# Kernel tuning notes

Measured on AMD Instinct MI355X. Metric: run time of the kernel, lower is better.

Reference implementation:

```python
import jax, jax.numpy as jnp
import numpy as np
import math

D_MODEL = 1024
NUM_HEADS = 16
D_K = D_MODEL // NUM_HEADS
B, NQ, NK = 2, 2048, 2048


def setup_inputs() -> dict:
    key = jax.random.key(0)
    ks = jax.random.split(key, 14)
    s = 1.0 / math.sqrt(D_MODEL)
    inp = {
        "query": jax.random.normal(ks[0], (B, NQ, D_MODEL), jnp.float32),
        "key": jax.random.normal(ks[1], (B, NK, D_MODEL), jnp.float32),
        "value": jax.random.normal(ks[2], (B, NK, D_MODEL), jnp.float32),
        "mask": jax.random.randint(ks[3], (B, NK), 0, 2, jnp.int32),
        "attn_bias": jax.random.normal(ks[4], (B, NQ, NK), jnp.float32),
        "w_q": jax.random.normal(ks[5], (D_MODEL, D_MODEL), jnp.float32) * s,
        "b_q": jnp.zeros((D_MODEL,), jnp.float32),
        "w_k": jax.random.normal(ks[6], (D_MODEL, D_MODEL), jnp.float32) * s,
        "b_k": jnp.zeros((D_MODEL,), jnp.float32),
        "w_v": jax.random.normal(ks[7], (D_MODEL, D_MODEL), jnp.float32) * s,
        "b_v": jnp.zeros((D_MODEL,), jnp.float32),
        "w_o": jax.random.normal(ks[8], (D_MODEL, D_MODEL), jnp.float32) * s,
        "b_o": jnp.zeros((D_MODEL,), jnp.float32),
    }
    return inp


def reference(query, key, value, mask, attn_bias, w_q, b_q, w_k, b_k, w_v, b_v, w_o, b_o):
    # Linear projections (torch Linear: x @ W^T + b), reshape to [B, H, N, d_k]
    def proj(x, w, b, n):
        return (x @ w.T + b).reshape(x.shape[0], n, NUM_HEADS, D_K).transpose(0, 2, 1, 3)

    Q = proj(query, w_q, b_q, query.shape[1])   # [B,H,Nq,dk]
    K = proj(key, w_k, b_k, key.shape[1])       # [B,H,Nk,dk]
    V = proj(value, w_v, b_v, value.shape[1])   # [B,H,Nk,dk]

    scores = jnp.einsum("bhqd,bhkd->bhqk", Q, K) / math.sqrt(D_K)
    scores = scores + attn_bias[:, None, :, :]           # bias broadcast over heads
    pad = (mask[:, None, None, :] == 0)                   # [B,1,1,Nk]
    scores = jnp.where(pad, jnp.float32(-1e9), scores)
    attn = jax.nn.softmax(scores, axis=-1)                # dropout is identity (eval)
    out = jnp.einsum("bhqk,bhkd->bhqd", attn, V)          # [B,H,Nq,dk]
    out = out.transpose(0, 2, 1, 3).reshape(query.shape[0], query.shape[1], D_MODEL)
    return out @ w_o.T + b_o
```

## Files before the change

kernel.cpp:

```cpp
#include <hip/hip_runtime.h>


typedef short bf16x8 __attribute__((ext_vector_type(8)));
typedef short bf16x4 __attribute__((ext_vector_type(4)));
typedef float f32x4 __attribute__((ext_vector_type(4)));
typedef int i32x4 __attribute__((ext_vector_type(4)));
typedef unsigned short u16;
typedef unsigned short u16x8 __attribute__((ext_vector_type(8)));
typedef unsigned short u16x4 __attribute__((ext_vector_type(4)));

#define MFMA16(a, b, c) __builtin_amdgcn_mfma_f32_16x16x32_bf16((a), (b), (c), 0, 0, 0)
#define GLD16(gp, lp)                                                     \
  __builtin_amdgcn_global_load_lds(                                       \
      (const __attribute__((address_space(1))) void*)(gp),                \
      (__attribute__((address_space(3))) void*)(lp), 16, 0, 0)

#define WAITVM_BAR(N) asm volatile("s_waitcnt vmcnt(" #N ")\ns_barrier" ::: "memory")
#define BAR() asm volatile("s_barrier" ::: "memory")

#if __has_builtin(__builtin_amdgcn_exp2f)
#define EXP2(x) __builtin_amdgcn_exp2f(x)
#else
#define EXP2(x) exp2f(x)
#endif

__device__ __forceinline__ f32x4 MFMA_PV(bf16x4 a, bf16x4 b, f32x4 c) {
#if __has_builtin(__builtin_amdgcn_mfma_f32_16x16x16bf16_1k)
  return __builtin_amdgcn_mfma_f32_16x16x16bf16_1k(a, b, c, 0, 0, 0);
#else
  asm("v_mfma_f32_16x16x16_bf16 %0, %1, %2, %0" : "+v"(c) : "v"(a), "v"(b));
  return c;
#endif
}

__device__ __forceinline__ u16 f2bf(float f) {
  union { float f; unsigned u; } v; v.f = f;
  return (u16)((v.u + 0x7fffu + ((v.u >> 16) & 1u)) >> 16);
}
__device__ __forceinline__ unsigned pk2(float x, float y) {
  union { float f; unsigned u; } a, b;
  a.f = x; b.f = y;
  return ((a.u + 0x8000u) >> 16) | ((b.u + 0x8000u) & 0xffff0000u);
}

struct ConvDesc { const float* src; u16* dst; int n; };
struct ConvArgs { ConvDesc d[7]; };

__device__ __forceinline__ void biasprep_body(const float* __restrict__ bias,
                                              const int* __restrict__ mask,
                                              u16* __restrict__ out, int i) {
  const int o0 = i * 16;
  const int rowg = o0 >> 11;
  const int b = rowg >> 11;
  const int off = o0 & 2047;
  const int a = off >> 6, g = (off >> 4) & 3;
  const float* src = bias + (size_t)rowg * 2048 + a * 64 + g * 4;
  const int* msk = mask + b * 2048 + a * 64 + g * 4;
  u16x8 w0 = {}, w1 = {};
#pragma unroll
  for (int c = 0; c < 4; c++) {
    f32x4 v = *(const f32x4*)(src + c * 16);
    i32x4 m = *(const i32x4*)(msk + c * 16);
#pragma unroll
    for (int j = 0; j < 4; j++) {
      u16 val = (m[j] != 0) ? f2bf(v[j] * 1.44269504f) : (u16)0xFF80;
      if (c < 2) w0[c * 4 + j] = val;
      else       w1[(c - 2) * 4 + j] = val;
    }
  }
  *(u16x8*)(out + o0) = w0;
  *(u16x8*)(out + o0 + 8) = w1;
}

__global__ __launch_bounds__(256)
void k_prep(ConvArgs a, const float* __restrict__ bias,
            const int* __restrict__ mask, u16* __restrict__ bout) {
  if (blockIdx.y == 7) {
    biasprep_body(bias, mask, bout, blockIdx.x * 256 + threadIdx.x);
    return;
  }
  ConvDesc cd = a.d[blockIdx.y];
  int i = (blockIdx.x * 256 + threadIdx.x) * 8;
  if (i >= cd.n) return;
  const float4* s = (const float4*)(cd.src + i);
  float4 f0 = s[0], f1 = s[1];
  u16x8 o;
  o[0] = f2bf(f0.x); o[1] = f2bf(f0.y); o[2] = f2bf(f0.z); o[3] = f2bf(f0.w);
  o[4] = f2bf(f1.x); o[5] = f2bf(f1.y); o[6] = f2bf(f1.z); o[7] = f2bf(f1.w);
  *(u16x8*)(cd.dst + i) = o;
}

__global__ __launch_bounds__(256)
void k_biasprep(const float* __restrict__ bias, const int* __restrict__ mask,
                u16* __restrict__ out) {
  biasprep_body(bias, mask, out, blockIdx.x * 256 + threadIdx.x);
}

template <int MF>
__device__ __forceinline__ void gemm_impl(const u16* __restrict__ A,
                                          const u16* __restrict__ Bw,
                                          const float* __restrict__ bias,
                                          void* __restrict__ outp, int mode,
                                          float oscale) {
  __shared__ u16 As[2][MF * 1024];
  __shared__ u16 Bs[2][4096];
  const int tid = threadIdx.x;
  const int lane = tid & 63;
  const int wv = tid >> 6;
  const int wr = wv >> 1, wc = wv & 1;
  const int m0 = blockIdx.y * (MF * 32), n0 = blockIdx.x * 128;

  f32x4 acc[MF][4] = {};

  const int s0 = tid, s1 = 256 + tid;
  const int r0 = s0 >> 2, c0 = (s0 & 3) ^ (r0 & 3);
  const int r1 = s1 >> 2, c1 = (s1 & 3) ^ (r1 & 3);
  const u16* gA0 = A + (size_t)(m0 + r0) * 1024 + c0 * 8;
  const u16* gA1 = A + (size_t)(m0 + r1) * 1024 + c1 * 8;
  const u16* gB0 = Bw + (size_t)(n0 + r0) * 1024 + c0 * 8;
  const u16* gB1 = Bw + (size_t)(n0 + r1) * 1024 + c1 * 8;
  u16* lA0 = &As[0][(tid & ~63) * 8];
  u16* lB0 = &Bs[0][(tid & ~63) * 8];

  GLD16(gA0, lA0);
  if constexpr (MF == 4) GLD16(gA1, lA0 + 2048);
  GLD16(gB0, lB0);
  GLD16(gB1, lB0 + 2048);
  WAITVM_BAR(0);

#define GSTEP(BUF, K0)                                                     \
  {                                                                        \
    const int nk = ((K0) + 32) & 1023;                                     \
    GLD16(gA0 + nk, lA0 + ((BUF) ^ 1) * (MF * 1024));                      \
    if constexpr (MF == 4)                                                 \
      GLD16(gA1 + nk, lA0 + 2048 + ((BUF) ^ 1) * (MF * 1024));             \
    GLD16(gB0 + nk, lB0 + ((BUF) ^ 1) * 4096);                             \
    GLD16(gB1 + nk, lB0 + 2048 + ((BUF) ^ 1) * 4096);                      \
    if constexpr (MF == 4) { WAITVM_BAR(4); } else { WAITVM_BAR(3); }      \
    bf16x8 af[MF], bfr[4];                                                 \
    _Pragma("unroll")                                                      \
    for (int mi = 0; mi < MF; mi++) {                                      \
      int row = wr * (MF * 16) + mi * 16 + (lane & 15);                    \
      int byt = row * 64 + (((lane >> 4) * 16) ^ ((row & 3) << 4));        \
      af[mi] = *(const bf16x8*)((const char*)&As[BUF][0] + byt);           \
    }                                                                      \
    _Pragma("unroll")                                                      \
    for (int ni = 0; ni < 4; ni++) {                                       \
      int row = wc * 64 + ni * 16 + (lane & 15);                           \
      int byt = row * 64 + (((lane >> 4) * 16) ^ ((row & 3) << 4));        \
      bfr[ni] = *(const bf16x8*)((const char*)&Bs[BUF][0] + byt);          \
    }                                                                      \
    __builtin_amdgcn_s_setprio(1);                                         \
    _Pragma("unroll")                                                      \
    for (int mi = 0; mi < MF; mi++)                                        \
      _Pragma("unroll")                                                    \
      for (int ni = 0; ni < 4; ni++)                                       \
        acc[mi][ni] = MFMA16(af[mi], bfr[ni], acc[mi][ni]);                \
    __builtin_amdgcn_s_setprio(0);                                         \
    BAR();                                                                 \
  }

  for (int k0 = 0; k0 < 1024; k0 += 64) {
    GSTEP(0, k0)
    GSTEP(1, k0 + 32)
  }
#undef GSTEP

#pragma unroll
  for (int ni = 0; ni < 4; ni++) {
    int n = n0 + wc * 64 + ni * 16 + (lane & 15);
    float bv = bias[n];
#pragma unroll
    for (int mi = 0; mi < MF; mi++) {
      int mb = m0 + wr * (MF * 16) + mi * 16 + (lane >> 4) * 4;
      if (mode == 2) {
        float* O = (float*)outp;
#pragma unroll
        for (int r = 0; r < 4; r++)
          O[(size_t)(mb + r) * 1024 + n] = (acc[mi][ni][r] + bv) * oscale;
      } else if (mode == 0) {
        u16* O = (u16*)outp;
        int b = mb >> 11, q = mb & 2047;
        int h = n >> 6, dk = n & 63;
        size_t base = ((size_t)(b * 16 + h) * 2048 + q) * 64 + dk;
#pragma unroll
        for (int r = 0; r < 4; r++)
          O[base + (size_t)r * 64] = f2bf((acc[mi][ni][r] + bv) * oscale);
      } else {
        u16* O = (u16*)outp;
        int b = mb >> 11, kv = mb & 2047;
        int h = n >> 6, dk = n & 63;
        u16x4 pk;
#pragma unroll
        for (int r = 0; r < 4; r++) pk[r] = f2bf((acc[mi][ni][r] + bv) * oscale);
        *(u16x4*)((u16*)O + ((size_t)((b * 16 + h) * 64 + dk)) * 2048 + kv) = pk;
      }
    }
  }
}

struct GemmDesc { const u16* A; const u16* W; const float* bias; void* out;
                  int mode; float oscale; };
struct Gemm3 { GemmDesc d[3]; };

__global__ __launch_bounds__(256, 2) void k_gemm_qkv(Gemm3 g3) {
  GemmDesc gd = g3.d[blockIdx.z];
  gemm_impl<4>(gd.A, gd.W, gd.bias, gd.out, gd.mode, gd.oscale);
}
__global__ __launch_bounds__(256, 2)
void k_gemm_o(const u16* __restrict__ A, const u16* __restrict__ W,
              const float* __restrict__ bias, float* __restrict__ out) {
  gemm_impl<2>(A, W, bias, out, 2, 1.0f);
}

__global__ __launch_bounds__(512, 4)
void k_attn(const u16* __restrict__ Qb, const u16* __restrict__ Kb,
            const u16* __restrict__ Vt, const u16* __restrict__ BiasE,
            u16* __restrict__ Ob) {
  __shared__ u16 Ks[2][128 * 64];
  __shared__ u16 Vs[2][64 * 128];

  const int tid = threadIdx.x, lane = tid & 63, w = tid >> 6;
  const int g = lane >> 4, q = lane & 15;
  const int bid = blockIdx.x;
  const int xcd = bid & 7, rr = bid >> 3;
  const int qt = rr & 15;
  const int pr = xcd + 8 * (rr >> 4);
  const int b = pr >> 4, h = pr & 15;
  const int q0 = qt * 128;
  const size_t bh = (size_t)(b * 16 + h);

  const u16* Qrow = Qb + (bh * 2048 + q0 + w * 16 + q) * 64;
  bf16x8 bq0 = *(const bf16x8*)(Qrow + g * 8);
  bf16x8 bq1 = *(const bf16x8*)(Qrow + 32 + g * 8);

  f32x4 acc[4] = {};
  float mrun = -1e30f, lrun = 0.f;

  const int sK1 = tid + 512;
  const int rK0 = tid >> 3, cK0 = (tid & 7) ^ (rK0 & 7);
  const int rK1 = sK1 >> 3, cK1 = (sK1 & 7) ^ (rK1 & 7);
  const int rV0 = tid >> 4, cV0 = (tid & 15) ^ (rV0 & 7);
  const int rV1 = sK1 >> 4, cV1 = (sK1 & 15) ^ (rV1 & 7);
  const u16* Kg = Kb + bh * 2048 * 64;
  const u16* Vg = Vt + bh * 64 * 2048;
  const int ld0 = (tid & ~63) * 8, ld1 = ld0 + 4096;

  const u16* brow = BiasE + ((size_t)b * 2048 + q0 + w * 16 + q) * 2048 + g * 16;

  GLD16(Kg + (size_t)rK0 * 64 + cK0 * 8, &Ks[0][ld0]);
  GLD16(Kg + (size_t)rK1 * 64 + cK1 * 8, &Ks[0][ld1]);
  GLD16(Vg + (size_t)rV0 * 2048 + cV0 * 8, &Vs[0][ld0]);
  GLD16(Vg + (size_t)rV1 * 2048 + cV1 * 8, &Vs[0][ld1]);
  u16x8 bb0 = *(const u16x8*)(brow);
  u16x8 bb1 = *(const u16x8*)(brow + 8);
  u16x8 bb2 = *(const u16x8*)(brow + 64);
  u16x8 bb3 = *(const u16x8*)(brow + 72);

#define ATTN_STEP(BUF, T)                                                      \
  {                                                                            \
    WAITVM_BAR(0);            \
    f32x4 sc[8];                                                               \
    __builtin_amdgcn_s_setprio(1);                                             \
    _Pragma("unroll")                                                          \
    for (int c = 0; c < 8; c++) {                                              \
      const int kvr = c * 16 + q;                                              \
      bf16x8 ak0 = *(const bf16x8*)((const char*)&Ks[BUF][0] + kvr * 128 +     \
                                    ((g * 16) ^ ((kvr & 7) << 4)));            \
      bf16x8 ak1 = *(const bf16x8*)((const char*)&Ks[BUF][0] + kvr * 128 +     \
                                    ((64 + g * 16) ^ ((kvr & 7) << 4)));       \
      const u16x8 blo = (c & 4) ? bb2 : bb0;                                   \
      const u16x8 bhi = (c & 4) ? bb3 : bb1;                                   \
      f32x4 cin;                                                               \
      _Pragma("unroll")                                                        \
      for (int r = 0; r < 4; r++) {                                            \
        unsigned braw = (unsigned)(((c & 3) < 2)                               \
                                       ? blo[(c & 3) * 4 + r]                  \
                                       : bhi[((c & 3) - 2) * 4 + r]);          \
        cin[r] = __uint_as_float(braw << 16);                                  \
      }                                                                        \
      f32x4 z = MFMA16(ak0, bq0, cin);                                         \
      sc[c] = MFMA16(ak1, bq1, z);                                             \
    }                                                                          \
    __builtin_amdgcn_s_setprio(0);                                             \
    const int nkv = (((T) + 1) & 15) * 128;                                    \
    GLD16(Kg + (size_t)(nkv + rK0) * 64 + cK0 * 8, &Ks[(BUF) ^ 1][ld0]);       \
    GLD16(Kg + (size_t)(nkv + rK1) * 64 + cK1 * 8, &Ks[(BUF) ^ 1][ld1]);       \
    GLD16(Vg + (size_t)rV0 * 2048 + nkv + cV0 * 8, &Vs[(BUF) ^ 1][ld0]);       \
    GLD16(Vg + (size_t)rV1 * 2048 + nkv + cV1 * 8, &Vs[(BUF) ^ 1][ld1]);       \
    bb0 = *(const u16x8*)(brow + nkv);                                         \
    bb1 = *(const u16x8*)(brow + nkv + 8);                                     \
    bb2 = *(const u16x8*)(brow + nkv + 64);                                    \
    bb3 = *(const u16x8*)(brow + nkv + 72);                                    \
    float tmax = -3e38f;                                                       \
    _Pragma("unroll")                                                          \
    for (int c = 0; c < 8; c++)                                                \
      _Pragma("unroll")                                                        \
      for (int r = 0; r < 4; r++) tmax = fmaxf(tmax, sc[c][r]);                \
    tmax = fmaxf(tmax, __shfl_xor(tmax, 16, 64));                              \
    tmax = fmaxf(tmax, __shfl_xor(tmax, 32, 64));                              \
    if (__any(tmax > mrun)) {                                                  \
      float mnew = fmaxf(mrun, tmax);                                          \
      float alpha = EXP2(mrun - mnew);                                         \
      mrun = mnew;                                                             \
      lrun *= alpha;                                                           \
      _Pragma("unroll")                                                        \
      for (int j = 0; j < 4; j++) {                                            \
        float aj = __shfl(alpha, g * 4 + j, 64);                               \
        _Pragma("unroll")                                                      \
        for (int d = 0; d < 4; d++) acc[d][j] *= aj;                           \
      }                                                                        \
    }                                                                          \
    float rsum = 0.f;                                                          \
    float pp[8][4];                                                            \
    _Pragma("unroll")                                                          \
    for (int c = 0; c < 8; c++)                                                \
      _Pragma("unroll")                                                        \
      for (int r = 0; r < 4; r++) {                                            \
        pp[c][r] = EXP2(sc[c][r] - mrun);                                      \
        rsum += pp[c][r];                                                      \
      }                                                                        \
    rsum += __shfl_xor(rsum, 16, 64);                                          \
    rsum += __shfl_xor(rsum, 32, 64);                                          \
    lrun += rsum;                                                              \
    __builtin_amdgcn_s_setprio(1);                                             \
    _Pragma("unroll")                                                          \
    for (int c = 0; c < 8; c++) {                                              \
      union { unsigned u[2]; bf16x4 v; } pa;                                   \
      pa.u[0] = pk2(pp[c][0], pp[c][1]);                                       \
      pa.u[1] = pk2(pp[c][2], pp[c][3]);                                       \
      _Pragma("unroll")                                                        \
      for (int d = 0; d < 4; d++) {                                            \
        const int dr = d * 16 + q;                                             \
        bf16x4 vb = *(const bf16x4*)((const char*)&Vs[BUF][0] + dr * 256 +     \
                                     ((c * 32 + g * 8) ^ ((dr & 7) << 4)));    \
        acc[d] = MFMA_PV(pa.v, vb, acc[d]);                                    \
      }                                                                        \
    }                                                                          \
    __builtin_amdgcn_s_setprio(0);                                             \
  }

  for (int t = 0; t < 16; t += 2) {
    ATTN_STEP(0, t)
    ATTN_STEP(1, t + 1)
  }
#undef ATTN_STEP

  float linv = 1.0f / lrun;
#pragma unroll
  for (int j = 0; j < 4; j++) {
    float li = __shfl(linv, g * 4 + j, 64);
    int qq = q0 + w * 16 + g * 4 + j;
#pragma unroll
    for (int d = 0; d < 4; d++)
      Ob[((size_t)b * 2048 + qq) * 1024 + h * 64 + d * 16 + q] =
          f2bf(acc[d][j] * li);
  }
}

extern "C" void kernel_launch(void* const* d_in, const int* in_sizes, int n_in,
                              void* d_out, int out_size, void* d_ws,
                              size_t ws_size, hipStream_t stream) {
  (void)in_sizes; (void)n_in; (void)out_size;
  const float* q_in = (const float*)d_in[0];
  const float* k_in = (const float*)d_in[1];
  const float* v_in = (const float*)d_in[2];
  const int* mask = (const int*)d_in[3];
  const float* attn_bias = (const float*)d_in[4];
  const float* w_q = (const float*)d_in[5];
  const float* b_q = (const float*)d_in[6];
  const float* w_k = (const float*)d_in[7];
  const float* b_k = (const float*)d_in[8];
  const float* w_v = (const float*)d_in[9];
  const float* b_v = (const float*)d_in[10];
  const float* w_o = (const float*)d_in[11];
  const float* b_o = (const float*)d_in[12];

  const size_t MB = 1u << 20;
  char* ws = (char*)d_ws;
  u16* XQ = (u16*)(ws + 0 * MB);
  u16* XK = (u16*)(ws + 8 * MB);
  u16* XV = (u16*)(ws + 16 * MB);
  u16* WQ = (u16*)(ws + 24 * MB);
  u16* WK = (u16*)(ws + 26 * MB);
  u16* WV = (u16*)(ws + 28 * MB);
  u16* WO = (u16*)(ws + 30 * MB);
  u16* Qb = (u16*)(ws + 32 * MB);
  u16* Kb = (u16*)(ws + 40 * MB);
  u16* Vt = (u16*)(ws + 48 * MB);
  u16* Ob = (u16*)(ws + 56 * MB);
  const bool merged = ws_size >= (size_t)80 * MB;
  u16* BiasE = (u16*)(ws + (merged ? 64 : 0) * MB);

  ConvArgs ca;
  ca.d[0] = {q_in, XQ, 4096 * 1024};
  ca.d[1] = {k_in, XK, 4096 * 1024};
  ca.d[2] = {v_in, XV, 4096 * 1024};
  ca.d[3] = {w_q, WQ, 1024 * 1024};
  ca.d[4] = {w_k, WK, 1024 * 1024};
  ca.d[5] = {w_v, WV, 1024 * 1024};
  ca.d[6] = {w_o, WO, 1024 * 1024};
  k_prep<<<dim3(2048, merged ? 8 : 7), 256, 0, stream>>>(ca, attn_bias, mask,
                                                         BiasE);

  const float QSCALE = 0.125f * 1.44269504f;
  Gemm3 g3;
  g3.d[0] = {XQ, WQ, b_q, (void*)Qb, 0, QSCALE};
  g3.d[1] = {XK, WK, b_k, (void*)Kb, 0, 1.0f};
  g3.d[2] = {XV, WV, b_v, (void*)Vt, 1, 1.0f};
  k_gemm_qkv<<<dim3(8, 32, 3), 256, 0, stream>>>(g3);

  if (!merged) k_biasprep<<<2048, 256, 0, stream>>>(attn_bias, mask, BiasE);

  k_attn<<<512, 512, 0, stream>>>(Qb, Kb, Vt, BiasE, Ob);

  k_gemm_o<<<dim3(8, 64), 256, 0, stream>>>(Ob, WO, b_o, (float*)d_out);
}
```

Baseline: 152.1 us.

## Switch attention kernel to 32x32x16 MFMA tiles with 4 waves per block

The attention kernel moves from 16x16 MFMA tiles to 32x32x16 bf16 MFMA. Each wave now owns 32 query rows, and the block shrinks to 256 threads. The P fragments are rearranged with v_permlane32_swap so they can feed the PV MFMA directly. The bias pre-layout is changed to match the new accumulator layout, and the output store is vectorized. This cuts cross-lane shuffles and LDS reads per FLOP, at the cost of more registers per wave and fewer waves per CU.

```diff
diff --git a/kernel.cpp b/kernel.cpp
--- a/kernel.cpp
+++ b/kernel.cpp
@@ -4,12 +4,14 @@
 typedef short bf16x8 __attribute__((ext_vector_type(8)));
 typedef short bf16x4 __attribute__((ext_vector_type(4)));
 typedef float f32x4 __attribute__((ext_vector_type(4)));
+typedef float f32x16 __attribute__((ext_vector_type(16)));
 typedef int i32x4 __attribute__((ext_vector_type(4)));
 typedef unsigned short u16;
 typedef unsigned short u16x8 __attribute__((ext_vector_type(8)));
 typedef unsigned short u16x4 __attribute__((ext_vector_type(4)));
 
 #define MFMA16(a, b, c) __builtin_amdgcn_mfma_f32_16x16x32_bf16((a), (b), (c), 0, 0, 0)
+#define MFMA32(a, b, c) __builtin_amdgcn_mfma_f32_32x32x16_bf16((a), (b), (c), 0, 0, 0)
 #define GLD16(gp, lp)                                                     \
   __builtin_amdgcn_global_load_lds(                                       \
       (const __attribute__((address_space(1))) void*)(gp),                \
@@ -24,15 +26,6 @@
 #define EXP2(x) exp2f(x)
 #endif
 
-__device__ __forceinline__ f32x4 MFMA_PV(bf16x4 a, bf16x4 b, f32x4 c) {
-#if __has_builtin(__builtin_amdgcn_mfma_f32_16x16x16bf16_1k)
-  return __builtin_amdgcn_mfma_f32_16x16x16bf16_1k(a, b, c, 0, 0, 0);
-#else
-  asm("v_mfma_f32_16x16x16_bf16 %0, %1, %2, %0" : "+v"(c) : "v"(a), "v"(b));
-  return c;
-#endif
-}
-
 __device__ __forceinline__ u16 f2bf(float f) {
   union { float f; unsigned u; } v; v.f = f;
   return (u16)((v.u + 0x7fffu + ((v.u >> 16) & 1u)) >> 16);
@@ -41,6 +34,9 @@
   union { float f; unsigned u; } a, b;
   a.f = x; b.f = y;
   return ((a.u + 0x8000u) >> 16) | ((b.u + 0x8000u) & 0xffff0000u);
+}
+__device__ __forceinline__ void pl32swap(unsigned& a, unsigned& b) {
+  asm("v_permlane32_swap_b32 %0, %1" : "+v"(a), "+v"(b));
 }
 
 struct ConvDesc { const float* src; u16* dst; int n; };
@@ -53,19 +49,20 @@
   const int rowg = o0 >> 11;
   const int b = rowg >> 11;
   const int off = o0 & 2047;
-  const int a = off >> 6, g = (off >> 4) & 3;
-  const float* src = bias + (size_t)rowg * 2048 + a * 64 + g * 4;
-  const int* msk = mask + b * 2048 + a * 64 + g * 4;
+  const int c = off >> 5;
+  const int hi = (off >> 4) & 1;
+  const float* src = bias + (size_t)rowg * 2048 + c * 32 + hi * 4;
+  const int* msk = mask + b * 2048 + c * 32 + hi * 4;
   u16x8 w0 = {}, w1 = {};
 #pragma unroll
-  for (int c = 0; c < 4; c++) {
-    f32x4 v = *(const f32x4*)(src + c * 16);
-    i32x4 m = *(const i32x4*)(msk + c * 16);
+  for (int t = 0; t < 4; t++) {
+    f32x4 v = *(const f32x4*)(src + t * 8);
+    i32x4 m = *(const i32x4*)(msk + t * 8);
 #pragma unroll
     for (int j = 0; j < 4; j++) {
       u16 val = (m[j] != 0) ? f2bf(v[j] * 1.44269504f) : (u16)0xFF80;
-      if (c < 2) w0[c * 4 + j] = val;
-      else       w1[(c - 2) * 4 + j] = val;
+      if (t < 2) w0[t * 4 + j] = val;
+      else       w1[(t - 2) * 4 + j] = val;
     }
   }
   *(u16x8*)(out + o0) = w0;
@@ -213,7 +210,7 @@
   gemm_impl<2>(A, W, bias, out, 2, 1.0f);
 }
 
-__global__ __launch_bounds__(512, 4)
+__global__ __launch_bounds__(256, 2)
 void k_attn(const u16* __restrict__ Qb, const u16* __restrict__ Kb,
             const u16* __restrict__ Vt, const u16* __restrict__ BiasE,
             u16* __restrict__ Ob) {
@@ -221,7 +218,7 @@
   __shared__ u16 Vs[2][64 * 128];
 
   const int tid = threadIdx.x, lane = tid & 63, w = tid >> 6;
-  const int g = lane >> 4, q = lane & 15;
+  const int l31 = lane & 31, hi2 = lane >> 5;
   const int bid = blockIdx.x;
   const int xcd = bid & 7, rr = bid >> 3;
   const int qt = rr & 15;
@@ -230,74 +227,87 @@
   const int q0 = qt * 128;
   const size_t bh = (size_t)(b * 16 + h);
 
-  const u16* Qrow = Qb + (bh * 2048 + q0 + w * 16 + q) * 64;
-  bf16x8 bq0 = *(const bf16x8*)(Qrow + g * 8);
-  bf16x8 bq1 = *(const bf16x8*)(Qrow + 32 + g * 8);
-
-  f32x4 acc[4] = {};
+  const u16* Qrow = Qb + (bh * 2048 + q0 + w * 32 + l31) * 64 + hi2 * 8;
+  bf16x8 bq[4];
+#pragma unroll
+  for (int dc = 0; dc < 4; dc++) bq[dc] = *(const bf16x8*)(Qrow + dc * 16);
+
+  f32x16 acc[2] = {};
   float mrun = -1e30f, lrun = 0.f;
 
-  const int sK1 = tid + 512;
-  const int rK0 = tid >> 3, cK0 = (tid & 7) ^ (rK0 & 7);
-  const int rK1 = sK1 >> 3, cK1 = (sK1 & 7) ^ (rK1 & 7);
-  const int rV0 = tid >> 4, cV0 = (tid & 15) ^ (rV0 & 7);
-  const int rV1 = sK1 >> 4, cV1 = (sK1 & 15) ^ (rV1 & 7);
   const u16* Kg = Kb + bh * 2048 * 64;
   const u16* Vg = Vt + bh * 64 * 2048;
-  const int ld0 = (tid & ~63) * 8, ld1 = ld0 + 4096;
-
-  const u16* brow = BiasE + ((size_t)b * 2048 + q0 + w * 16 + q) * 2048 + g * 16;
-
-  GLD16(Kg + (size_t)rK0 * 64 + cK0 * 8, &Ks[0][ld0]);
-  GLD16(Kg + (size_t)rK1 * 64 + cK1 * 8, &Ks[0][ld1]);
-  GLD16(Vg + (size_t)rV0 * 2048 + cV0 * 8, &Vs[0][ld0]);
-  GLD16(Vg + (size_t)rV1 * 2048 + cV1 * 8, &Vs[0][ld1]);
-  u16x8 bb0 = *(const u16x8*)(brow);
-  u16x8 bb1 = *(const u16x8*)(brow + 8);
-  u16x8 bb2 = *(const u16x8*)(brow + 64);
-  u16x8 bb3 = *(const u16x8*)(brow + 72);
+  int rK[4], cK[4], rV[4], cV[4], ldd[4];
+#pragma unroll
+  for (int i = 0; i < 4; i++) {
+    int s = i * 256 + tid;
+    rK[i] = s >> 3; cK[i] = (s & 7) ^ (rK[i] & 7);
+    rV[i] = s >> 4; cV[i] = (s & 15) ^ (rV[i] & 7);
+    ldd[i] = (i * 256 + (tid & ~63)) * 8;
+  }
+  const int kx = (lane & 7) << 4;
+
+  const u16* brow =
+      BiasE + ((size_t)b * 2048 + q0 + w * 32 + l31) * 2048 + hi2 * 16;
+
+#pragma unroll
+  for (int i = 0; i < 4; i++)
+    GLD16(Kg + (size_t)rK[i] * 64 + cK[i] * 8, &Ks[0][ldd[i]]);
+#pragma unroll
+  for (int i = 0; i < 4; i++)
+    GLD16(Vg + (size_t)rV[i] * 2048 + cV[i] * 8, &Vs[0][ldd[i]]);
+  u16x8 bb[4][2];
+#pragma unroll
+  for (int c = 0; c < 4; c++) {
+    bb[c][0] = *(const u16x8*)(brow + c * 32);
+    bb[c][1] = *(const u16x8*)(brow + c * 32 + 8);
+  }
 
 #define ATTN_STEP(BUF, T)                                                      \
   {                                                                            \
     WAITVM_BAR(0);            \
-    f32x4 sc[8];                                                               \
+    const char* kb = (const char*)&Ks[BUF][0];                                 \
+    const char* vb = (const char*)&Vs[BUF][0];                                 \
+    f32x16 sc[4];                                                              \
     __builtin_amdgcn_s_setprio(1);                                             \
     _Pragma("unroll")                                                          \
-    for (int c = 0; c < 8; c++) {                                              \
-      const int kvr = c * 16 + q;                                              \
-      bf16x8 ak0 = *(const bf16x8*)((const char*)&Ks[BUF][0] + kvr * 128 +     \
-                                    ((g * 16) ^ ((kvr & 7) << 4)));            \
-      bf16x8 ak1 = *(const bf16x8*)((const char*)&Ks[BUF][0] + kvr * 128 +     \
-                                    ((64 + g * 16) ^ ((kvr & 7) << 4)));       \
-      const u16x8 blo = (c & 4) ? bb2 : bb0;                                   \
-      const u16x8 bhi = (c & 4) ? bb3 : bb1;                                   \
-      f32x4 cin;                                                               \
-      _Pragma("unroll")                                                        \
-      for (int r = 0; r < 4; r++) {                                            \
-        unsigned braw = (unsigned)(((c & 3) < 2)                               \
-                                       ? blo[(c & 3) * 4 + r]                  \
-                                       : bhi[((c & 3) - 2) * 4 + r]);          \
-        cin[r] = __uint_as_float(braw << 16);                                  \
+    for (int c = 0; c < 4; c++) {                                              \
+      f32x16 z;                                                                \
+      _Pragma("unroll")                                                        \
+      for (int r = 0; r < 8; r++)                                              \
+        z[r] = __uint_as_float((unsigned)bb[c][0][r] << 16);                   \
+      _Pragma("unroll")                                                        \
+      for (int r = 0; r < 8; r++)                                              \
+        z[8 + r] = __uint_as_float((unsigned)bb[c][1][r] << 16);               \
+      const int rowb = (c * 32 + l31) * 128;                                   \
+      _Pragma("unroll")                                                        \
+      for (int dc = 0; dc < 4; dc++) {                                         \
+        bf16x8 ak =                                                            \
+            *(const bf16x8*)(kb + rowb + ((dc * 32 + hi2 * 16) ^ kx));         \
+        z = MFMA32(ak, bq[dc], z);                                             \
       }                                                                        \
-      f32x4 z = MFMA16(ak0, bq0, cin);                                         \
-      sc[c] = MFMA16(ak1, bq1, z);                                             \
+      sc[c] = z;                                                               \
     }                                                                          \
     __builtin_amdgcn_s_setprio(0);                                             \
     const int nkv = (((T) + 1) & 15) * 128;                                    \
-    GLD16(Kg + (size_t)(nkv + rK0) * 64 + cK0 * 8, &Ks[(BUF) ^ 1][ld0]);       \
-    GLD16(Kg + (size_t)(nkv + rK1) * 64 + cK1 * 8, &Ks[(BUF) ^ 1][ld1]);       \
-    GLD16(Vg + (size_t)rV0 * 2048 + nkv + cV0 * 8, &Vs[(BUF) ^ 1][ld0]);       \
-    GLD16(Vg + (size_t)rV1 * 2048 + nkv + cV1 * 8, &Vs[(BUF) ^ 1][ld1]);       \
-    bb0 = *(const u16x8*)(brow + nkv);                                         \
-    bb1 = *(const u16x8*)(brow + nkv + 8);                                     \
-    bb2 = *(const u16x8*)(brow + nkv + 64);                                    \
-    bb3 = *(const u16x8*)(brow + nkv + 72);                                    \
+    _Pragma("unroll")                                                          \
+    for (int i = 0; i < 4; i++)                                                \
+      GLD16(Kg + (size_t)(nkv + rK[i]) * 64 + cK[i] * 8,                       \
+            &Ks[(BUF) ^ 1][ldd[i]]);                                           \
+    _Pragma("unroll")                                                          \
+    for (int i = 0; i < 4; i++)                                                \
+      GLD16(Vg + (size_t)rV[i] * 2048 + nkv + cV[i] * 8,                       \
+            &Vs[(BUF) ^ 1][ldd[i]]);                                           \
+    _Pragma("unroll")                                                          \
+    for (int c = 0; c < 4; c++) {                                              \
+      bb[c][0] = *(const u16x8*)(brow + nkv + c * 32);                         \
+      bb[c][1] = *(const u16x8*)(brow + nkv + c * 32 + 8);                     \
+    }                                                                          \
     float tmax = -3e38f;                                                       \
     _Pragma("unroll")                                                          \
-    for (int c = 0; c < 8; c++)                                                \
-      _Pragma("unroll")                                                        \
-      for (int r = 0; r < 4; r++) tmax = fmaxf(tmax, sc[c][r]);                \
-    tmax = fmaxf(tmax, __shfl_xor(tmax, 16, 64));                              \
+    for (int c = 0; c < 4; c++)                                                \
+      _Pragma("unroll")                                                        \
+      for (int r = 0; r < 16; r++) tmax = fmaxf(tmax, sc[c][r]);               \
     tmax = fmaxf(tmax, __shfl_xor(tmax, 32, 64));                              \
     if (__any(tmax > mrun)) {                                                  \
       float mnew = fmaxf(mrun, tmax);                                          \
@@ -305,36 +315,41 @@
       mrun = mnew;                                                             \
       lrun *= alpha;                                                           \
       _Pragma("unroll")                                                        \
-      for (int j = 0; j < 4; j++) {                                            \
-        float aj = __shfl(alpha, g * 4 + j, 64);                               \
+      for (int ds = 0; ds < 2; ds++)                                           \
         _Pragma("unroll")                                                      \
-        for (int d = 0; d < 4; d++) acc[d][j] *= aj;                           \
-      }                                                                        \
+        for (int r = 0; r < 16; r++) acc[ds][r] *= alpha;                      \
     }                                                                          \
     float rsum = 0.f;                                                          \
-    float pp[8][4];                                                            \
-    _Pragma("unroll")                                                          \
-    for (int c = 0; c < 8; c++)                                                \
-      _Pragma("unroll")                                                        \
-      for (int r = 0; r < 4; r++) {                                            \
-        pp[c][r] = EXP2(sc[c][r] - mrun);                                      \
-        rsum += pp[c][r];                                                      \
+    _Pragma("unroll")                                                          \
+    for (int c = 0; c < 4; c++)                                                \
+      _Pragma("unroll")                                                        \
+      for (int r = 0; r < 16; r++) {                                           \
+        sc[c][r] = EXP2(sc[c][r] - mrun);                                      \
+        rsum += sc[c][r];                                                      \
       }                                                                        \
-    rsum += __shfl_xor(rsum, 16, 64);                                          \
     rsum += __shfl_xor(rsum, 32, 64);                                          \
     lrun += rsum;                                                              \
     __builtin_amdgcn_s_setprio(1);                                             \
     _Pragma("unroll")                                                          \
-    for (int c = 0; c < 8; c++) {                                              \
-      union { unsigned u[2]; bf16x4 v; } pa;                                   \
-      pa.u[0] = pk2(pp[c][0], pp[c][1]);                                       \
-      pa.u[1] = pk2(pp[c][2], pp[c][3]);                                       \
-      _Pragma("unroll")                                                        \
-      for (int d = 0; d < 4; d++) {                                            \
-        const int dr = d * 16 + q;                                             \
-        bf16x4 vb = *(const bf16x4*)((const char*)&Vs[BUF][0] + dr * 256 +     \
-                                     ((c * 32 + g * 8) ^ ((dr & 7) << 4)));    \
-        acc[d] = MFMA_PV(pa.v, vb, acc[d]);                                    \
+    for (int c = 0; c < 4; c++) {                                              \
+      unsigned a0 = pk2(sc[c][0], sc[c][1]), b0 = pk2(sc[c][4], sc[c][5]);     \
+      unsigned a1 = pk2(sc[c][2], sc[c][3]), b1 = pk2(sc[c][6], sc[c][7]);     \
+      unsigned e0 = pk2(sc[c][8], sc[c][9]), f0 = pk2(sc[c][12], sc[c][13]);   \
+      unsigned e1 = pk2(sc[c][10], sc[c][11]), f1 = pk2(sc[c][14], sc[c][15]); \
+      pl32swap(a0, b0); pl32swap(a1, b1);                                      \
+      pl32swap(e0, f0); pl32swap(e1, f1);                                      \
+      union { unsigned u[4]; bf16x8 v; } fe, fo;                               \
+      fe.u[0] = a0; fe.u[1] = a1; fe.u[2] = b0; fe.u[3] = b1;                  \
+      fo.u[0] = e0; fo.u[1] = e1; fo.u[2] = f0; fo.u[3] = f1;                  \
+      _Pragma("unroll")                                                        \
+      for (int ds = 0; ds < 2; ds++) {                                         \
+        const int vrow = (ds * 32 + l31) * 256;                                \
+        bf16x8 ve =                                                            \
+            *(const bf16x8*)(vb + vrow + (((c * 4 + hi2) * 16) ^ kx));         \
+        acc[ds] = MFMA32(ve, fe.v, acc[ds]);                                   \
+        bf16x8 vo =                                                            \
+            *(const bf16x8*)(vb + vrow + (((c * 4 + 2 + hi2) * 16) ^ kx));     \
+        acc[ds] = MFMA32(vo, fo.v, acc[ds]);                                   \
       }                                                                        \
     }                                                                          \
     __builtin_amdgcn_s_setprio(0);                                             \
@@ -347,15 +362,17 @@
 #undef ATTN_STEP
 
   float linv = 1.0f / lrun;
-#pragma unroll
-  for (int j = 0; j < 4; j++) {
-    float li = __shfl(linv, g * 4 + j, 64);
-    int qq = q0 + w * 16 + g * 4 + j;
-#pragma unroll
-    for (int d = 0; d < 4; d++)
-      Ob[((size_t)b * 2048 + qq) * 1024 + h * 64 + d * 16 + q] =
-          f2bf(acc[d][j] * li);
-  }
+  const size_t obase =
+      ((size_t)b * 2048 + q0 + w * 32 + l31) * 1024 + h * 64 + hi2 * 4;
+#pragma unroll
+  for (int ds = 0; ds < 2; ds++)
+#pragma unroll
+    for (int t = 0; t < 4; t++) {
+      u16x4 pk;
+#pragma unroll
+      for (int j = 0; j < 4; j++) pk[j] = f2bf(acc[ds][t * 4 + j] * linv);
+      *(u16x4*)(Ob + obase + ds * 32 + t * 8) = pk;
+    }
 }
 
 extern "C" void kernel_launch(void* const* d_in, const int* in_sizes, int n_in,
@@ -412,7 +429,7 @@
 
   if (!merged) k_biasprep<<<2048, 256, 0, stream>>>(attn_bias, mask, BiasE);
 
-  k_attn<<<512, 512, 0, stream>>>(Qb, Kb, Vt, BiasE, Ob);
+  k_attn<<<512, 256, 0, stream>>>(Qb, Kb, Vt, BiasE, Ob);
 
   k_gemm_o<<<dim3(8, 64), 256, 0, stream>>>(Ob, WO, b_o, (float*)d_out);
 }
```

Measured after the change: 149.3 us. About the same (-1.8%).
